# Performance work log

Hardware: AMD Instinct MI355X
Metric: run time of the kernel (lower is better)

Reference implementation:

```python
import jax, jax.numpy as jnp
import numpy as np

EMBD_DIM = 512
HIDDEN_DIM = 512
TARGET_DIM = 128
BATCH = 64
MAX_SET = 2048


def setup_inputs() -> dict:
    key = jax.random.key(0)
    ks = jax.random.split(key, 10)
    E, H, T = EMBD_DIM, HIDDEN_DIM, TARGET_DIM
    s = lambda fan_in: 1.0 / np.sqrt(fan_in)
    return {
        "words": jax.random.normal(ks[0], (BATCH, MAX_SET, E), dtype=jnp.float32),
        # attention_layer: Linear(2E -> H) followed by tanh; v: (H, 1)
        "W_att": jax.random.uniform(ks[1], (2 * E, H), jnp.float32, -s(2 * E), s(2 * E)),
        "b_att": jax.random.uniform(ks[2], (H,), jnp.float32, -s(2 * E), s(2 * E)),
        "v": jax.random.normal(ks[3], (H, 1), dtype=jnp.float32),
        # pred_net: Linear(E,H) -> ReLU -> Linear(H,H) -> ReLU -> Linear(H,T)
        "W1": jax.random.uniform(ks[4], (E, H), jnp.float32, -s(E), s(E)),
        "b1": jax.random.uniform(ks[5], (H,), jnp.float32, -s(E), s(E)),
        "W2": jax.random.uniform(ks[6], (H, H), jnp.float32, -s(H), s(H)),
        "b2": jax.random.uniform(ks[7], (H,), jnp.float32, -s(H), s(H)),
        "W3": jax.random.uniform(ks[8], (H, T), jnp.float32, -s(H), s(H)),
        "b3": jax.random.uniform(ks[9], (T,), jnp.float32, -s(H), s(H)),
    }


def reference(words, W_att, b_att, v, W1, b1, W2, b2, W3, b3):
    # words: [B, S, E]. A row is "valid" iff its feature-sum is nonzero
    # (matches words.sum(2).abs().sign() in the torch code).
    mask = jnp.sign(jnp.abs(words.sum(-1)))           # [B, S], 0/1 float
    lengths = mask.sum(axis=1, keepdims=True)          # [B, 1]
    # context = mean over valid rows (padded rows are exactly zero)
    context = words.sum(axis=1, keepdims=True) / lengths[..., None]  # [B, 1, E]
    context = jnp.broadcast_to(context, words.shape)   # [B, S, E]

    x = jnp.concatenate([words, context], axis=-1)     # [B, S, 2E]
    h = jnp.tanh(x @ W_att + b_att)                    # [B, S, H]
    scores = (h @ v)[..., 0]                           # [B, S]

    # per-segment softmax over valid rows only (masked_select + per-batch
    # Softmax in the original == masked softmax here)
    scores = jnp.where(mask > 0, scores, jnp.full_like(scores, -1e30))
    attn = jax.nn.softmax(scores, axis=1)              # [B, S]

    rep = jnp.einsum("bs,bse->be", attn, words)        # [B, E]

    pred = jax.nn.relu(rep @ W1 + b1)
    pred = jax.nn.relu(pred @ W2 + b2)
    pred = pred @ W3 + b3                              # [B, T]
    return pred
```

## Files before the change

kernel.cpp:

```cpp
#include <hip/hip_runtime.h>
#include <hip/hip_bf16.h>
#include <hip/hip_fp16.h>
#include <math.h>

#define B 64
#define S 2048
#define E 512
#define HD 512
#define TD 128
#define M_TOT (B*S)

#define OFF_MASK   0
#define OFF_CTXP   (OFF_MASK + B*S)
#define OFF_LENP   (OFF_CTXP + 8*B*E)
#define OFF_CB     (OFF_LENP + 8*B)
#define OFF_SC     (OFF_CB + B*HD)
#define OFF_SMAX   (OFF_SC + B*S)
#define OFF_SDEN   (OFF_SMAX + B)
#define OFF_REPP   (OFF_SDEN + B)
#define OFF_H1     (OFF_REPP + 8*B*E)
#define OFF_H2     (OFF_H1 + B*HD)
#define OFF_SCP    (OFF_H2 + B*HD)
#define OFF_WPK    (OFF_SCP + 2*B*S)

typedef __attribute__((ext_vector_type(8))) short short8;
typedef __attribute__((ext_vector_type(4))) float f32x4;

__device__ inline unsigned int f2hu(float x) {
    __half h = __float2half(x);
    unsigned short u; __builtin_memcpy(&u, &h, 2); return (unsigned int)u;
}

__device__ inline float fast_tanh(float x) {
    float a = fabsf(x);
    float e = __expf(-2.0f * a);
    float r = (1.0f - e) / (1.0f + e);
    return copysignf(r, x);
}

__global__ __launch_bounds__(256)
void k0_pack(const float* __restrict__ W_att, unsigned short* __restrict__ Wpk)
{
    int tid = blockIdx.x*256 + threadIdx.x;
    int e = tid >> 9, h = tid & 511;
    float w = W_att[(size_t)e*HD + h];
    int kstep = e >> 5, kb = (e >> 3) & 3, j = e & 7, f = h >> 4, l15 = h & 15;
    size_t dst = ((((size_t)kstep*32 + f)*64) + kb*16 + l15)*8 + j;
    Wpk[dst] = (unsigned short)f2hu(w);
}

__global__ __launch_bounds__(256)
void k1_maskcol(const float* __restrict__ words, float* __restrict__ mask,
                float* __restrict__ ctxp, float* __restrict__ lenp)
{
    int bid = blockIdx.x;
    int b = bid >> 3, ch = bid & 7;
    int t = threadIdx.x;
    int w = t >> 6, l = t & 63;
    __shared__ __align__(16) float colred[4][E];
    __shared__ float lenred[4];
    const float* base = words + (size_t)(b * S + ch * 256) * E;
    float4 c0 = make_float4(0.f,0.f,0.f,0.f), c1 = make_float4(0.f,0.f,0.f,0.f);
    float wlen = 0.0f;
    for (int r = w; r < 256; r += 4) {
        const float* row = base + (size_t)r * E;
        float4 a  = *(const float4*)(row + 4*l);
        float4 bb = *(const float4*)(row + 256 + 4*l);
        float rs = a.x+a.y+a.z+a.w + bb.x+bb.y+bb.z+bb.w;
        #pragma unroll
        for (int m = 1; m < 64; m <<= 1) rs += __shfl_xor(rs, m);
        c0.x += a.x;  c0.y += a.y;  c0.z += a.z;  c0.w += a.w;
        c1.x += bb.x; c1.y += bb.y; c1.z += bb.z; c1.w += bb.w;
        if (l == 0) {
            float mv = (rs != 0.0f) ? 1.0f : 0.0f;
            mask[(size_t)b*S + ch*256 + r] = mv;
            wlen += mv;
        }
    }
    *(float4*)&colred[w][4*l]       = c0;
    *(float4*)&colred[w][256 + 4*l] = c1;
    if (l == 0) lenred[w] = wlen;
    __syncthreads();
    float s1 = colred[0][t]+colred[1][t]+colred[2][t]+colred[3][t];
    float s2 = colred[0][t+256]+colred[1][t+256]+colred[2][t+256]+colred[3][t+256];
    size_t o = ((size_t)ch * B + b) * E;
    ctxp[o + t]       = s1;
    ctxp[o + t + 256] = s2;
    if (t == 0) lenp[ch*B + b] = lenred[0]+lenred[1]+lenred[2]+lenred[3];
}

__global__ __launch_bounds__(256)
void k2_cb(const float* __restrict__ W_att, const float* __restrict__ b_att,
           const float* __restrict__ ctxp, const float* __restrict__ lenp,
           float* __restrict__ cb)
{
    int bid = blockIdx.x;
    int b = bid >> 1, hc = bid & 1;
    int t = threadIdx.x;
    __shared__ float ctxL[E];
    float len = 0.f;
    #pragma unroll
    for (int k = 0; k < 8; ++k) len += lenp[k*B + b];
    float inv = 1.0f / len;
    for (int c = t; c < E; c += 256) {
        float sv = 0.f;
        #pragma unroll
        for (int k = 0; k < 8; ++k) sv += ctxp[((size_t)k*B + b)*E + c];
        ctxL[c] = sv * inv;
    }
    __syncthreads();
    int h = hc*256 + t;
    const float* Wb = W_att + (size_t)E * HD;
    float a0 = b_att[h], a1 = 0.f, a2 = 0.f, a3 = 0.f;
    #pragma unroll 4
    for (int e = 0; e < E; e += 4) {
        a0 += ctxL[e]   * Wb[(size_t)e*HD + h];
        a1 += ctxL[e+1] * Wb[(size_t)(e+1)*HD + h];
        a2 += ctxL[e+2] * Wb[(size_t)(e+2)*HD + h];
        a3 += ctxL[e+3] * Wb[(size_t)(e+3)*HD + h];
    }
    cb[(size_t)b*HD + h] = (a0 + a1) + (a2 + a3);
}

__global__ __launch_bounds__(512, 4)
void k3_scores(const float* __restrict__ words,
               const unsigned short* __restrict__ Wpk,
               const float* __restrict__ cb, const float* __restrict__ v,
               float* __restrict__ scp)
{
    __shared__ __align__(16) unsigned char smem[16384];
    int bid = blockIdx.x;
    int mt = bid >> 1, nc = bid & 1;
    int m0 = mt * 128;
    int b  = m0 >> 11;
    int t = threadIdx.x;
    int lane = t & 63, wid = t >> 6;
    int wr = wid >> 2, wc = wid & 3;

    f32x4 acc[4][4];
    #pragma unroll
    for (int i = 0; i < 4; ++i)
        #pragma unroll
        for (int j = 0; j < 4; ++j) acc[i][j] = (f32x4)0.0f;

    int r = t >> 2, kq = t & 3;
    const float* aSrc = words + (size_t)(m0 + r)*E + kq*8;
    int abase = (r >> 4)*1024 + kq*256 + (r & 15)*16;

    float4 pA[2];
    const unsigned short* bBase = Wpk + (((size_t)(nc*16 + wc*4))*64 + lane)*8;

#define LOADA(ks) do { \
        const float* _s = aSrc + (ks)*32; \
        pA[0] = *(const float4*)(_s); pA[1] = *(const float4*)(_s+4); } while(0)

#define STAGEA(buf) do { \
        float xs[8] = {pA[0].x,pA[0].y,pA[0].z,pA[0].w, pA[1].x,pA[1].y,pA[1].z,pA[1].w}; \
        unsigned int uw[4]; \
        _Pragma("unroll") \
        for (int p = 0; p < 4; ++p) \
            uw[p] = f2hu(xs[2*p]) | (f2hu(xs[2*p+1]) << 16); \
        *(uint4*)&(buf)[abase] = make_uint4(uw[0],uw[1],uw[2],uw[3]); } while(0)

#define LDB(ks,cf) (*(const short8*)(bBase + ((size_t)(ks)*32 + (cf))*512))

    LOADA(0);
    STAGEA(smem);
    LOADA(1);
    short8 bcur[4];
    #pragma unroll
    for (int cf = 0; cf < 4; ++cf) bcur[cf] = LDB(0, cf);
    __syncthreads();

    for (int k = 0; k < 16; ++k) {
        unsigned char* bufc = smem + (k & 1)*8192;
        unsigned char* bufn = smem + ((k & 1) ^ 1)*8192;

        short8 ah[4];
        #pragma unroll
        for (int rf = 0; rf < 4; ++rf)
            ah[rf] = *(const short8*)&bufc[(wr*4 + rf)*1024 + lane*16];

        if (k < 15) STAGEA(bufn);
        if (k < 14) LOADA(k + 2);

        #pragma unroll
        for (int cf = 0; cf < 4; ++cf) {
            #pragma unroll
            for (int rf = 0; rf < 4; ++rf)
                acc[rf][cf] = __builtin_amdgcn_mfma_f32_16x16x32_f16(ah[rf], bcur[cf], acc[rf][cf], 0, 0, 0);
            if (k < 15) bcur[cf] = LDB(k + 1, cf);
        }
        __syncthreads();
    }

    float ssum[4][4];
    #pragma unroll
    for (int i = 0; i < 4; ++i)
        #pragma unroll
        for (int rr = 0; rr < 4; ++rr) ssum[i][rr] = 0.f;

    #pragma unroll
    for (int cf = 0; cf < 4; ++cf) {
        int col = nc*256 + wc*64 + cf*16 + (lane & 15);
        float cbv = cb[(size_t)b*HD + col];
        float vv  = v[col];
        #pragma unroll
        for (int rf = 0; rf < 4; ++rf)
            #pragma unroll
            for (int rr = 0; rr < 4; ++rr)
                ssum[rf][rr] += fast_tanh(acc[rf][cf][rr] + cbv) * vv;
    }
    #pragma unroll
    for (int m = 1; m < 16; m <<= 1)
        #pragma unroll
        for (int rf = 0; rf < 4; ++rf)
            #pragma unroll
            for (int rr = 0; rr < 4; ++rr)
                ssum[rf][rr] += __shfl_xor(ssum[rf][rr], m);

    float* scr = (float*)smem;
    if ((lane & 15) == 0) {
        #pragma unroll
        for (int rf = 0; rf < 4; ++rf)
            #pragma unroll
            for (int rr = 0; rr < 4; ++rr)
                scr[wc*128 + wr*64 + rf*16 + (lane >> 4)*4 + rr] = ssum[rf][rr];
    }
    __syncthreads();
    if (t < 128) {
        float val = (scr[t] + scr[128 + t]) + (scr[256 + t] + scr[384 + t]);
        scp[(size_t)nc*M_TOT + m0 + t] = val;
    }
#undef LOADA
#undef STAGEA
#undef LDB
}

__global__ __launch_bounds__(256)
void k4a_softstats(const float* __restrict__ scp, const float* __restrict__ mask,
                   float* __restrict__ sc, float* __restrict__ smax, float* __restrict__ sden)
{
    int b = blockIdx.x, t = threadIdx.x;
    __shared__ float red[256];
    float xs[8];
    float mx = -1e30f;
    #pragma unroll
    for (int k = 0; k < 8; ++k) {
        size_t m = (size_t)b*S + t + 256*k;
        float x = scp[m] + scp[(size_t)M_TOT + m];
        float mk = mask[m];
        x = (mk > 0.0f) ? x : -1e30f;
        sc[m] = x;
        xs[k] = x; mx = fmaxf(mx, x);
    }
    red[t] = mx; __syncthreads();
    for (int off = 128; off > 0; off >>= 1) {
        if (t < off) red[t] = fmaxf(red[t], red[t+off]);
        __syncthreads();
    }
    float gmax = red[0]; __syncthreads();
    float se = 0.f;
    #pragma unroll
    for (int k = 0; k < 8; ++k) se += expf(xs[k] - gmax);
    red[t] = se; __syncthreads();
    for (int off = 128; off > 0; off >>= 1) {
        if (t < off) red[t] += red[t+off];
        __syncthreads();
    }
    if (t == 0) { smax[b] = gmax; sden[b] = red[0]; }
}

__global__ __launch_bounds__(256)
void k4b_rep(const float* __restrict__ words, const float* __restrict__ sc,
             const float* __restrict__ smax, const float* __restrict__ sden,
             float* __restrict__ repp)
{
    int bid = blockIdx.x;
    int b = bid >> 3, ch = bid & 7;
    int t = threadIdx.x;
    __shared__ float wrow[256];
    int s = ch*256 + t;
    wrow[t] = expf(sc[(size_t)b*S + s] - smax[b]) / sden[b];
    __syncthreads();
    const float* base = words + (size_t)(b*S + ch*256)*E + 2*t;
    float2 acc = make_float2(0.f, 0.f);
    #pragma unroll 4
    for (int r = 0; r < 256; ++r) {
        float2 wv = *(const float2*)(base + (size_t)r*E);
        float a = wrow[r];
        acc.x = fmaf(a, wv.x, acc.x);
        acc.y = fmaf(a, wv.y, acc.y);
    }
    size_t o = ((size_t)ch*B + b)*E + 2*t;
    *(float2*)&repp[o] = acc;
}

__global__ __launch_bounds__(256)
void k5a_l1(const float* __restrict__ repp, const float* __restrict__ W1,
            const float* __restrict__ b1, float* __restrict__ h1)
{
    int bid = blockIdx.x;
    int b = bid >> 1, hc = bid & 1;
    int t = threadIdx.x;
    __shared__ float repL[E];
    for (int c = t; c < E; c += 256) {
        float sv = 0.f;
        #pragma unroll
        for (int k = 0; k < 8; ++k) sv += repp[((size_t)k*B + b)*E + c];
        repL[c] = sv;
    }
    __syncthreads();
    int h = hc*256 + t;
    float a0 = b1[h], a1 = 0.f, a2 = 0.f, a3 = 0.f;
    #pragma unroll 4
    for (int e = 0; e < E; e += 4) {
        a0 += repL[e]   * W1[(size_t)e*HD + h];
        a1 += repL[e+1] * W1[(size_t)(e+1)*HD + h];
        a2 += repL[e+2] * W1[(size_t)(e+2)*HD + h];
        a3 += repL[e+3] * W1[(size_t)(e+3)*HD + h];
    }
    h1[(size_t)b*HD + h] = fmaxf((a0 + a1) + (a2 + a3), 0.f);
}

__global__ __launch_bounds__(256)
void k5b_l2(const float* __restrict__ h1, const float* __restrict__ W2,
            const float* __restrict__ b2, float* __restrict__ h2)
{
    int bid = blockIdx.x;
    int b = bid >> 1, hc = bid & 1;
    int t = threadIdx.x;
    __shared__ float inL[HD];
    for (int c = t; c < HD; c += 256) inL[c] = h1[(size_t)b*HD + c];
    __syncthreads();
    int h = hc*256 + t;
    float a0 = b2[h], a1 = 0.f, a2 = 0.f, a3 = 0.f;
    #pragma unroll 4
    for (int e = 0; e < HD; e += 4) {
        a0 += inL[e]   * W2[(size_t)e*HD + h];
        a1 += inL[e+1] * W2[(size_t)(e+1)*HD + h];
        a2 += inL[e+2] * W2[(size_t)(e+2)*HD + h];
        a3 += inL[e+3] * W2[(size_t)(e+3)*HD + h];
    }
    h2[(size_t)b*HD + h] = fmaxf((a0 + a1) + (a2 + a3), 0.f);
}

__global__ __launch_bounds__(128)
void k5c_l3(const float* __restrict__ h2, const float* __restrict__ W3,
            const float* __restrict__ b3, float* __restrict__ out)
{
    int b = blockIdx.x;
    int t = threadIdx.x;
    __shared__ float inL[HD];
    for (int c = t; c < HD; c += 128) inL[c] = h2[(size_t)b*HD + c];
    __syncthreads();
    float a0 = b3[t], a1 = 0.f, a2 = 0.f, a3 = 0.f;
    #pragma unroll 4
    for (int e = 0; e < HD; e += 4) {
        a0 += inL[e]   * W3[(size_t)e*TD + t];
        a1 += inL[e+1] * W3[(size_t)(e+1)*TD + t];
        a2 += inL[e+2] * W3[(size_t)(e+2)*TD + t];
        a3 += inL[e+3] * W3[(size_t)(e+3)*TD + t];
    }
    out[(size_t)b*TD + t] = (a0 + a1) + (a2 + a3);
}

extern "C" void kernel_launch(void* const* d_in, const int* in_sizes, int n_in,
                              void* d_out, int out_size, void* d_ws, size_t ws_size,
                              hipStream_t stream)
{
    const float* words = (const float*)d_in[0];
    const float* W_att = (const float*)d_in[1];
    const float* b_att = (const float*)d_in[2];
    const float* v     = (const float*)d_in[3];
    const float* W1    = (const float*)d_in[4];
    const float* b1    = (const float*)d_in[5];
    const float* W2    = (const float*)d_in[6];
    const float* b2    = (const float*)d_in[7];
    const float* W3    = (const float*)d_in[8];
    const float* b3    = (const float*)d_in[9];
    (void)in_sizes; (void)n_in; (void)out_size; (void)ws_size;

    float* ws   = (float*)d_ws;
    float* mask = ws + OFF_MASK;
    float* ctxp = ws + OFF_CTXP;
    float* lenp = ws + OFF_LENP;
    float* cb   = ws + OFF_CB;
    float* sc   = ws + OFF_SC;
    float* smax = ws + OFF_SMAX;
    float* sden = ws + OFF_SDEN;
    float* repp = ws + OFF_REPP;
    float* h1   = ws + OFF_H1;
    float* h2   = ws + OFF_H2;
    float* scp  = ws + OFF_SCP;
    unsigned short* Wpk = (unsigned short*)(ws + OFF_WPK);
    float* out  = (float*)d_out;

    hipLaunchKernelGGL(k0_pack,      dim3(1024), dim3(256), 0, stream, W_att, Wpk);
    hipLaunchKernelGGL(k1_maskcol,   dim3(B*8),  dim3(256), 0, stream, words, mask, ctxp, lenp);
    hipLaunchKernelGGL(k2_cb,        dim3(B*2),  dim3(256), 0, stream, W_att, b_att, ctxp, lenp, cb);
    hipLaunchKernelGGL(k3_scores,    dim3(2048), dim3(512), 0, stream, words, Wpk, cb, v, scp);
    hipLaunchKernelGGL(k4a_softstats,dim3(B),    dim3(256), 0, stream, scp, mask, sc, smax, sden);
    hipLaunchKernelGGL(k4b_rep,      dim3(B*8),  dim3(256), 0, stream, words, sc, smax, sden, repp);
    hipLaunchKernelGGL(k5a_l1,       dim3(B*2),  dim3(256), 0, stream, repp, W1, b1, h1);
    hipLaunchKernelGGL(k5b_l2,       dim3(B*2),  dim3(256), 0, stream, h1, W2, b2, h2);
    hipLaunchKernelGGL(k5c_l3,       dim3(B),    dim3(128), 0, stream, h2, W3, b3, out);
}
```

Measured before the change: 288.7 us.

## Cache fp16 copy of words in first pass; fuse softmax/rep and MLP kernels

The mask/column-sum pass now also writes an fp16 copy of the words tensor to workspace when it is large enough. The scores GEMM and the attention-weighted sum then read this half-size copy instead of re-reading and converting fp32. The softmax stats are merged into the rep kernel, each block recomputing the per-batch max and sum, and the three MLP layers become one kernel. This trades an extra 128MB write for two half-size reads. The rep sum now uses fp16-rounded words, and the fast path depends on the workspace size.

Measured after the change: 313.4 us. +8.6%, slower.

```diff
diff --git a/kernel.cpp b/kernel.cpp
--- a/kernel.cpp
+++ b/kernel.cpp
@@ -14,21 +14,22 @@
 #define OFF_CTXP   (OFF_MASK + B*S)
 #define OFF_LENP   (OFF_CTXP + 8*B*E)
 #define OFF_CB     (OFF_LENP + 8*B)
-#define OFF_SC     (OFF_CB + B*HD)
-#define OFF_SMAX   (OFF_SC + B*S)
-#define OFF_SDEN   (OFF_SMAX + B)
-#define OFF_REPP   (OFF_SDEN + B)
-#define OFF_H1     (OFF_REPP + 8*B*E)
-#define OFF_H2     (OFF_H1 + B*HD)
-#define OFF_SCP    (OFF_H2 + B*HD)
+#define OFF_REPP   (OFF_CB + B*HD)
+#define OFF_SCP    (OFF_REPP + 8*B*E)
 #define OFF_WPK    (OFF_SCP + 2*B*S)
+#define OFF_WH     (OFF_WPK + 131072)
+#define WS_NEED_FLOATS ((size_t)OFF_WH + (size_t)B*S*E/2)
 
 typedef __attribute__((ext_vector_type(8))) short short8;
 typedef __attribute__((ext_vector_type(4))) float f32x4;
+typedef __attribute__((ext_vector_type(4))) unsigned short ushort4_t;
 
 __device__ inline unsigned int f2hu(float x) {
     __half h = __float2half(x);
     unsigned short u; __builtin_memcpy(&u, &h, 2); return (unsigned int)u;
+}
+__device__ inline float hu2f(unsigned short u) {
+    __half h; __builtin_memcpy(&h, &u, 2); return __half2float(h);
 }
 
 __device__ inline float fast_tanh(float x) {
@@ -49,9 +50,11 @@
     Wpk[dst] = (unsigned short)f2hu(w);
 }
 
+template<bool WRITE_H>
 __global__ __launch_bounds__(256)
 void k1_maskcol(const float* __restrict__ words, float* __restrict__ mask,
-                float* __restrict__ ctxp, float* __restrict__ lenp)
+                float* __restrict__ ctxp, float* __restrict__ lenp,
+                unsigned short* __restrict__ wordsH)
 {
     int bid = blockIdx.x;
     int b = bid >> 3, ch = bid & 7;
@@ -60,12 +63,22 @@
     __shared__ __align__(16) float colred[4][E];
     __shared__ float lenred[4];
     const float* base = words + (size_t)(b * S + ch * 256) * E;
+    unsigned short* hbase = wordsH + (size_t)(b * S + ch * 256) * E;
     float4 c0 = make_float4(0.f,0.f,0.f,0.f), c1 = make_float4(0.f,0.f,0.f,0.f);
     float wlen = 0.0f;
     for (int r = w; r < 256; r += 4) {
         const float* row = base + (size_t)r * E;
         float4 a  = *(const float4*)(row + 4*l);
         float4 bb = *(const float4*)(row + 256 + 4*l);
+        if (WRITE_H) {
+            ushort4_t ha, hb;
+            ha[0]=(unsigned short)f2hu(a.x);  ha[1]=(unsigned short)f2hu(a.y);
+            ha[2]=(unsigned short)f2hu(a.z);  ha[3]=(unsigned short)f2hu(a.w);
+            hb[0]=(unsigned short)f2hu(bb.x); hb[1]=(unsigned short)f2hu(bb.y);
+            hb[2]=(unsigned short)f2hu(bb.z); hb[3]=(unsigned short)f2hu(bb.w);
+            *(ushort4_t*)(hbase + (size_t)r*E + 4*l)       = ha;
+            *(ushort4_t*)(hbase + (size_t)r*E + 256 + 4*l) = hb;
+        }
         float rs = a.x+a.y+a.z+a.w + bb.x+bb.y+bb.z+bb.w;
         #pragma unroll
         for (int m = 1; m < 64; m <<= 1) rs += __shfl_xor(rs, m);
@@ -122,8 +135,10 @@
     cb[(size_t)b*HD + h] = (a0 + a1) + (a2 + a3);
 }
 
+template<bool F16>
 __global__ __launch_bounds__(512, 4)
 void k3_scores(const float* __restrict__ words,
+               const unsigned short* __restrict__ wordsH,
                const unsigned short* __restrict__ Wpk,
                const float* __restrict__ cb, const float* __restrict__ v,
                float* __restrict__ scp)
@@ -144,24 +159,35 @@
         for (int j = 0; j < 4; ++j) acc[i][j] = (f32x4)0.0f;
 
     int r = t >> 2, kq = t & 3;
-    const float* aSrc = words + (size_t)(m0 + r)*E + kq*8;
+    const float* aSrcF = words + (size_t)(m0 + r)*E + kq*8;
+    const unsigned short* aSrcH = wordsH + (size_t)(m0 + r)*E + kq*8;
     int abase = (r >> 4)*1024 + kq*256 + (r & 15)*16;
 
-    float4 pA[2];
+    float4 pF[2];
+    uint4  pH;
+
+    auto LOADA = [&](int ks) {
+        if constexpr (F16) {
+            pH = *(const uint4*)(aSrcH + ks*32);
+        } else {
+            const float* _s = aSrcF + ks*32;
+            pF[0] = *(const float4*)(_s); pF[1] = *(const float4*)(_s+4);
+        }
+    };
+    auto STAGEA = [&](unsigned char* buf) {
+        if constexpr (F16) {
+            *(uint4*)&buf[abase] = pH;
+        } else {
+            float xs[8] = {pF[0].x,pF[0].y,pF[0].z,pF[0].w, pF[1].x,pF[1].y,pF[1].z,pF[1].w};
+            unsigned int uw[4];
+            #pragma unroll
+            for (int p = 0; p < 4; ++p)
+                uw[p] = f2hu(xs[2*p]) | (f2hu(xs[2*p+1]) << 16);
+            *(uint4*)&buf[abase] = make_uint4(uw[0],uw[1],uw[2],uw[3]);
+        }
+    };
+
     const unsigned short* bBase = Wpk + (((size_t)(nc*16 + wc*4))*64 + lane)*8;
-
-#define LOADA(ks) do { \
-        const float* _s = aSrc + (ks)*32; \
-        pA[0] = *(const float4*)(_s); pA[1] = *(const float4*)(_s+4); } while(0)
-
-#define STAGEA(buf) do { \
-        float xs[8] = {pA[0].x,pA[0].y,pA[0].z,pA[0].w, pA[1].x,pA[1].y,pA[1].z,pA[1].w}; \
-        unsigned int uw[4]; \
-        _Pragma("unroll") \
-        for (int p = 0; p < 4; ++p) \
-            uw[p] = f2hu(xs[2*p]) | (f2hu(xs[2*p+1]) << 16); \
-        *(uint4*)&(buf)[abase] = make_uint4(uw[0],uw[1],uw[2],uw[3]); } while(0)
-
 #define LDB(ks,cf) (*(const short8*)(bBase + ((size_t)(ks)*32 + (cf))*512))
 
     LOADA(0);
@@ -232,26 +258,28 @@
         float val = (scr[t] + scr[128 + t]) + (scr[256 + t] + scr[384 + t]);
         scp[(size_t)nc*M_TOT + m0 + t] = val;
     }
-#undef LOADA
-#undef STAGEA
 #undef LDB
 }
 
+template<bool F16>
 __global__ __launch_bounds__(256)
-void k4a_softstats(const float* __restrict__ scp, const float* __restrict__ mask,
-                   float* __restrict__ sc, float* __restrict__ smax, float* __restrict__ sden)
-{
-    int b = blockIdx.x, t = threadIdx.x;
+void k4_rep(const float* __restrict__ words, const unsigned short* __restrict__ wordsH,
+            const float* __restrict__ scp, const float* __restrict__ mask,
+            float* __restrict__ repp)
+{
+    int bid = blockIdx.x;
+    int b = bid >> 3, ch = bid & 7;
+    int t = threadIdx.x;
     __shared__ float red[256];
+    __shared__ float wrow[256];
+
     float xs[8];
     float mx = -1e30f;
     #pragma unroll
     for (int k = 0; k < 8; ++k) {
-        size_t m = (size_t)b*S + t + 256*k;
+        size_t m = (size_t)b*S + 256*k + t;
         float x = scp[m] + scp[(size_t)M_TOT + m];
-        float mk = mask[m];
-        x = (mk > 0.0f) ? x : -1e30f;
-        sc[m] = x;
+        x = (mask[m] > 0.0f) ? x : -1e30f;
         xs[k] = x; mx = fmaxf(mx, x);
     }
     red[t] = mx; __syncthreads();
@@ -268,101 +296,94 @@
         if (t < off) red[t] += red[t+off];
         __syncthreads();
     }
-    if (t == 0) { smax[b] = gmax; sden[b] = red[0]; }
-}
-
-__global__ __launch_bounds__(256)
-void k4b_rep(const float* __restrict__ words, const float* __restrict__ sc,
-             const float* __restrict__ smax, const float* __restrict__ sden,
-             float* __restrict__ repp)
-{
-    int bid = blockIdx.x;
-    int b = bid >> 3, ch = bid & 7;
-    int t = threadIdx.x;
-    __shared__ float wrow[256];
-    int s = ch*256 + t;
-    wrow[t] = expf(sc[(size_t)b*S + s] - smax[b]) / sden[b];
-    __syncthreads();
-    const float* base = words + (size_t)(b*S + ch*256)*E + 2*t;
+    float den = red[0];
+    wrow[t] = expf(xs[ch] - gmax) / den;
+    __syncthreads();
+
     float2 acc = make_float2(0.f, 0.f);
-    #pragma unroll 4
-    for (int r = 0; r < 256; ++r) {
-        float2 wv = *(const float2*)(base + (size_t)r*E);
-        float a = wrow[r];
-        acc.x = fmaf(a, wv.x, acc.x);
-        acc.y = fmaf(a, wv.y, acc.y);
+    if (F16) {
+        const unsigned short* base = wordsH + (size_t)(b*S + ch*256)*E + 2*t;
+        #pragma unroll 4
+        for (int rr = 0; rr < 256; ++rr) {
+            unsigned int u = *(const unsigned int*)(base + (size_t)rr*E);
+            float a = wrow[rr];
+            acc.x = fmaf(a, hu2f((unsigned short)(u & 0xffff)), acc.x);
+            acc.y = fmaf(a, hu2f((unsigned short)(u >> 16)),    acc.y);
+        }
+    } else {
+        const float* base = words + (size_t)(b*S + ch*256)*E + 2*t;
+        #pragma unroll 4
+        for (int rr = 0; rr < 256; ++rr) {
+            float2 wv = *(const float2*)(base + (size_t)rr*E);
+            float a = wrow[rr];
+            acc.x = fmaf(a, wv.x, acc.x);
+            acc.y = fmaf(a, wv.y, acc.y);
+        }
     }
     size_t o = ((size_t)ch*B + b)*E + 2*t;
     *(float2*)&repp[o] = acc;
 }
 
 __global__ __launch_bounds__(256)
-void k5a_l1(const float* __restrict__ repp, const float* __restrict__ W1,
-            const float* __restrict__ b1, float* __restrict__ h1)
-{
-    int bid = blockIdx.x;
-    int b = bid >> 1, hc = bid & 1;
+void k5_mlp(const float* __restrict__ repp,
+            const float* __restrict__ W1, const float* __restrict__ b1,
+            const float* __restrict__ W2, const float* __restrict__ b2,
+            const float* __restrict__ W3, const float* __restrict__ b3,
+            float* __restrict__ out)
+{
+    int b = blockIdx.x;
     int t = threadIdx.x;
-    __shared__ float repL[E];
+    __shared__ float xL[HD];
+    __shared__ float yL[HD];
     for (int c = t; c < E; c += 256) {
         float sv = 0.f;
         #pragma unroll
         for (int k = 0; k < 8; ++k) sv += repp[((size_t)k*B + b)*E + c];
-        repL[c] = sv;
-    }
-    __syncthreads();
-    int h = hc*256 + t;
-    float a0 = b1[h], a1 = 0.f, a2 = 0.f, a3 = 0.f;
-    #pragma unroll 4
-    for (int e = 0; e < E; e += 4) {
-        a0 += repL[e]   * W1[(size_t)e*HD + h];
-        a1 += repL[e+1] * W1[(size_t)(e+1)*HD + h];
-        a2 += repL[e+2] * W1[(size_t)(e+2)*HD + h];
-        a3 += repL[e+3] * W1[(size_t)(e+3)*HD + h];
-    }
-    h1[(size_t)b*HD + h] = fmaxf((a0 + a1) + (a2 + a3), 0.f);
-}
-
-__global__ __launch_bounds__(256)
-void k5b_l2(const float* __restrict__ h1, const float* __restrict__ W2,
-            const float* __restrict__ b2, float* __restrict__ h2)
-{
-    int bid = blockIdx.x;
-    int b = bid >> 1, hc = bid & 1;
-    int t = threadIdx.x;
-    __shared__ float inL[HD];
-    for (int c = t; c < HD; c += 256) inL[c] = h1[(size_t)b*HD + c];
-    __syncthreads();
-    int h = hc*256 + t;
-    float a0 = b2[h], a1 = 0.f, a2 = 0.f, a3 = 0.f;
-    #pragma unroll 4
-    for (int e = 0; e < HD; e += 4) {
-        a0 += inL[e]   * W2[(size_t)e*HD + h];
-        a1 += inL[e+1] * W2[(size_t)(e+1)*HD + h];
-        a2 += inL[e+2] * W2[(size_t)(e+2)*HD + h];
-        a3 += inL[e+3] * W2[(size_t)(e+3)*HD + h];
-    }
-    h2[(size_t)b*HD + h] = fmaxf((a0 + a1) + (a2 + a3), 0.f);
-}
-
-__global__ __launch_bounds__(128)
-void k5c_l3(const float* __restrict__ h2, const float* __restrict__ W3,
-            const float* __restrict__ b3, float* __restrict__ out)
-{
-    int b = blockIdx.x;
-    int t = threadIdx.x;
-    __shared__ float inL[HD];
-    for (int c = t; c < HD; c += 128) inL[c] = h2[(size_t)b*HD + c];
-    __syncthreads();
-    float a0 = b3[t], a1 = 0.f, a2 = 0.f, a3 = 0.f;
-    #pragma unroll 4
-    for (int e = 0; e < HD; e += 4) {
-        a0 += inL[e]   * W3[(size_t)e*TD + t];
-        a1 += inL[e+1] * W3[(size_t)(e+1)*TD + t];
-        a2 += inL[e+2] * W3[(size_t)(e+2)*TD + t];
-        a3 += inL[e+3] * W3[(size_t)(e+3)*TD + t];
-    }
-    out[(size_t)b*TD + t] = (a0 + a1) + (a2 + a3);
+        xL[c] = sv;
+    }
+    __syncthreads();
+    #pragma unroll
+    for (int oo = 0; oo < 2; ++oo) {
+        int h = oo*256 + t;
+        float a0 = b1[h], a1 = 0.f, a2 = 0.f, a3 = 0.f;
+        #pragma unroll 4
+        for (int e = 0; e < E; e += 4) {
+            a0 += xL[e]   * W1[(size_t)e*HD + h];
+            a1 += xL[e+1] * W1[(size_t)(e+1)*HD + h];
+            a2 += xL[e+2] * W1[(size_t)(e+2)*HD + h];
+            a3 += xL[e+3] * W1[(size_t)(e+3)*HD + h];
+        }
+        yL[h] = fmaxf((a0 + a1) + (a2 + a3), 0.f);
+    }
+    __syncthreads();
+    float l2v[2];
+    #pragma unroll
+    for (int oo = 0; oo < 2; ++oo) {
+        int h = oo*256 + t;
+        float a0 = b2[h], a1 = 0.f, a2 = 0.f, a3 = 0.f;
+        #pragma unroll 4
+        for (int e = 0; e < HD; e += 4) {
+            a0 += yL[e]   * W2[(size_t)e*HD + h];
+            a1 += yL[e+1] * W2[(size_t)(e+1)*HD + h];
+            a2 += yL[e+2] * W2[(size_t)(e+2)*HD + h];
+            a3 += yL[e+3] * W2[(size_t)(e+3)*HD + h];
+        }
+        l2v[oo] = fmaxf((a0 + a1) + (a2 + a3), 0.f);
+    }
+    __syncthreads();
+    xL[t] = l2v[0]; xL[256 + t] = l2v[1];
+    __syncthreads();
+    if (t < TD) {
+        float a0 = b3[t], a1 = 0.f, a2 = 0.f, a3 = 0.f;
+        #pragma unroll 4
+        for (int e = 0; e < HD; e += 4) {
+            a0 += xL[e]   * W3[(size_t)e*TD + t];
+            a1 += xL[e+1] * W3[(size_t)(e+1)*TD + t];
+            a2 += xL[e+2] * W3[(size_t)(e+2)*TD + t];
+            a3 += xL[e+3] * W3[(size_t)(e+3)*TD + t];
+        }
+        out[(size_t)b*TD + t] = (a0 + a1) + (a2 + a3);
+    }
 }
 
 extern "C" void kernel_launch(void* const* d_in, const int* in_sizes, int n_in,
@@ -379,30 +400,34 @@
     const float* b2    = (const float*)d_in[7];
     const float* W3    = (const float*)d_in[8];
     const float* b3    = (const float*)d_in[9];
-    (void)in_sizes; (void)n_in; (void)out_size; (void)ws_size;
+    (void)in_sizes; (void)n_in; (void)out_size;
 
     float* ws   = (float*)d_ws;
     float* mask = ws + OFF_MASK;
     float* ctxp = ws + OFF_CTXP;
     float* lenp = ws + OFF_LENP;
     float* cb   = ws + OFF_CB;
-    float* sc   = ws + OFF_SC;
-    float* smax = ws + OFF_SMAX;
-    float* sden = ws + OFF_SDEN;
     float* repp = ws + OFF_REPP;
-    float* h1   = ws + OFF_H1;
-    float* h2   = ws + OFF_H2;
     float* scp  = ws + OFF_SCP;
-    unsigned short* Wpk = (unsigned short*)(ws + OFF_WPK);
+    unsigned short* Wpk    = (unsigned short*)(ws + OFF_WPK);
+    unsigned short* wordsH = (unsigned short*)(ws + OFF_WH);
     float* out  = (float*)d_out;
 
-    hipLaunchKernelGGL(k0_pack,      dim3(1024), dim3(256), 0, stream, W_att, Wpk);
-    hipLaunchKernelGGL(k1_maskcol,   dim3(B*8),  dim3(256), 0, stream, words, mask, ctxp, lenp);
-    hipLaunchKernelGGL(k2_cb,        dim3(B*2),  dim3(256), 0, stream, W_att, b_att, ctxp, lenp, cb);
-    hipLaunchKernelGGL(k3_scores,    dim3(2048), dim3(512), 0, stream, words, Wpk, cb, v, scp);
-    hipLaunchKernelGGL(k4a_softstats,dim3(B),    dim3(256), 0, stream, scp, mask, sc, smax, sden);
-    hipLaunchKernelGGL(k4b_rep,      dim3(B*8),  dim3(256), 0, stream, words, sc, smax, sden, repp);
-    hipLaunchKernelGGL(k5a_l1,       dim3(B*2),  dim3(256), 0, stream, repp, W1, b1, h1);
-    hipLaunchKernelGGL(k5b_l2,       dim3(B*2),  dim3(256), 0, stream, h1, W2, b2, h2);
-    hipLaunchKernelGGL(k5c_l3,       dim3(B),    dim3(128), 0, stream, h2, W3, b3, out);
-}
+    bool useF16 = ws_size >= WS_NEED_FLOATS * sizeof(float);
+
+    hipLaunchKernelGGL(k0_pack, dim3(1024), dim3(256), 0, stream, W_att, Wpk);
+    if (useF16) {
+        hipLaunchKernelGGL(k1_maskcol<true>,  dim3(B*8), dim3(256), 0, stream, words, mask, ctxp, lenp, wordsH);
+    } else {
+        hipLaunchKernelGGL(k1_maskcol<false>, dim3(B*8), dim3(256), 0, stream, words, mask, ctxp, lenp, wordsH);
+    }
+    hipLaunchKernelGGL(k2_cb, dim3(B*2), dim3(256), 0, stream, W_att, b_att, ctxp, lenp, cb);
+    if (useF16) {
+        hipLaunchKernelGGL(k3_scores<true>,  dim3(2048), dim3(512), 0, stream, words, wordsH, Wpk, cb, v, scp);
+        hipLaunchKernelGGL(k4_rep<true>,     dim3(B*8),  dim3(256), 0, stream, words, wordsH, scp, mask, repp);
+    } else {
+        hipLaunchKernelGGL(k3_scores<false>, dim3(2048), dim3(512), 0, stream, words, wordsH, Wpk, cb, v, scp);
+        hipLaunchKernelGGL(k4_rep<false>,    dim3(B*8),  dim3(256), 0, stream, words, wordsH, scp, mask, repp);
+    }
+    hipLaunchKernelGGL(k5_mlp, dim3(B), dim3(256), 0, stream, repp, W1, b1, W2, b2, W3, b3, out);
+}
```
